# Kernel tuning notes

Measured on AMD Instinct MI355X. Metric: run time of the kernel, lower is better.

The kernel has to match this reference:

```python
import jax, jax.numpy as jnp
import numpy as np

# Static module config (matches init_kwargs)
DIM = 192
NHEADS = 6
WH, WW = 4, 8
SH, SW = 2, 4
MLP_HID = int(DIM * 4.0)


def _relative_position_index(wh, ww):
    ch, cw = np.meshgrid(np.arange(wh), np.arange(ww), indexing='ij')
    coords = np.stack([ch, cw]).reshape(2, -1)  # [2, wh*ww]
    rel = coords[:, :, None] - coords[:, None, :]  # [2, N, N]
    rel = rel.transpose(1, 2, 0)
    rel[:, :, 0] += wh - 1
    rel[:, :, 1] += ww - 1
    rel[:, :, 0] *= 2 * ww - 1
    return rel.sum(-1)  # [N, N] int


def _attn_mask(H, W, wh, ww, sh, sw):
    # Swin shift mask: -100 where tokens come from different shifted regions.
    img = np.zeros((H, W), dtype=np.float32)
    cnt = 0
    hs = (slice(0, -sh), slice(-sh, None)) if sh > 0 else (slice(0, H),)
    ws = (slice(0, -sw), slice(-sw, None)) if sw > 0 else (slice(0, W),)
    for h in hs:
        for w in ws:
            img[h, w] = cnt
            cnt += 1
    nwh, nww = H // wh, W // ww
    mw = img.reshape(nwh, wh, nww, ww).transpose(0, 2, 1, 3).reshape(-1, wh * ww)
    diff = mw[:, None, :] - mw[:, :, None]  # [nW, N, N]
    return np.where(diff != 0, -100.0, 0.0).astype(np.float32)


def _layernorm(x, g, b, eps=1e-5):
    mu = x.mean(-1, keepdims=True)
    var = ((x - mu) ** 2).mean(-1, keepdims=True)
    return (x - mu) * jax.lax.rsqrt(var + eps) * g + b


def setup_inputs() -> dict:
    key = jax.random.key(0)
    ks = jax.random.split(key, 12)
    B, H, W, C = 8, 64, 512, DIM
    x = jax.random.normal(ks[0], (B, H * W, C), dtype=jnp.float32)
    s = 0.02
    return {
        'x': x, 'H': H, 'W': W,
        'g1': jnp.ones((C,), jnp.float32), 'be1': jnp.zeros((C,), jnp.float32),
        'w_qkv': jax.random.normal(ks[1], (C, 3 * C), jnp.float32) * s,
        'b_qkv': jnp.zeros((3 * C,), jnp.float32),
        'w_proj': jax.random.normal(ks[2], (C, C), jnp.float32) * s,
        'b_proj': jnp.zeros((C,), jnp.float32),
        'bias_table': jax.random.normal(ks[3], ((2 * WH - 1) * (2 * WW - 1), NHEADS), jnp.float32) * s,
        'g2': jnp.ones((C,), jnp.float32), 'be2': jnp.zeros((C,), jnp.float32),
        'w1': jax.random.normal(ks[4], (C, MLP_HID), jnp.float32) * s,
        'bm1': jnp.zeros((MLP_HID,), jnp.float32),
        'w2': jax.random.normal(ks[5], (MLP_HID, C), jnp.float32) * s,
        'bm2': jnp.zeros((C,), jnp.float32),
    }


def reference(x, H, W, g1, be1, w_qkv, b_qkv, w_proj, b_proj, bias_table, g2, be2, w1, bm1, w2, bm2):
    B, Ntok, C = x.shape
    hd = C // NHEADS
    scale = hd ** -0.5
    N = WH * WW
    nwh, nww = H // WH, W // WW
    nW = nwh * nww

    # --- shifted window partition ---
    xr = x.reshape(B, H, W, C)
    shifted = jnp.roll(xr, (-SH, -SW), axis=(1, 2))
    win = shifted.reshape(B, nwh, WH, nww, WW, C).transpose(0, 1, 3, 2, 4, 5)
    win = win.reshape(B * nW, N, C)

    # --- window attention on norm1(windows) ---
    wn = _layernorm(win, g1, be1)
    qkv = (wn @ w_qkv + b_qkv).reshape(B * nW, N, 3, NHEADS, hd)
    q = qkv[:, :, 0].transpose(0, 2, 1, 3)  # [Bn, h, N, d]
    k = qkv[:, :, 1].transpose(0, 2, 1, 3)
    v = qkv[:, :, 2].transpose(0, 2, 1, 3)
    attn = jnp.einsum('bhnd,bhmd->bhnm', q, k) * scale

    rel_idx = _relative_position_index(WH, WW)  # static numpy
    bias = bias_table[rel_idx.reshape(-1)].reshape(N, N, NHEADS).transpose(2, 0, 1)
    attn = attn + bias[None]

    mask = jnp.asarray(_attn_mask(H, W, WH, WW, SH, SW))  # [nW, N, N]
    attn = attn.reshape(B, nW, NHEADS, N, N) + mask[None, :, None]
    attn = jax.nn.softmax(attn.reshape(B * nW, NHEADS, N, N), axis=-1)

    out = jnp.einsum('bhnm,bhmd->bhnd', attn, v)
    out = out.transpose(0, 2, 1, 3).reshape(B * nW, N, C)
    out = out @ w_proj + b_proj

    # --- window reverse + unshift ---
    merged = out.reshape(B, nwh, nww, WH, WW, C).transpose(0, 1, 3, 2, 4, 5).reshape(B, H, W, C)
    x_attn = jnp.roll(merged, (SH, SW), axis=(1, 2)).reshape(B, Ntok, C)

    x1 = x + x_attn
    h = _layernorm(x1, g2, be2)
    mlp = jax.nn.gelu(h @ w1 + bm1, approximate=False) @ w2 + bm2
    return x1 + mlp
```

## Files before the change

kernel.cpp:

```cpp
#include <hip/hip_runtime.h>
#include <hip/hip_bf16.h>

typedef unsigned short u16;
typedef unsigned int u32;
typedef __attribute__((ext_vector_type(8))) short short8;
typedef __attribute__((ext_vector_type(4))) float f32x4;

#define DEVFN static __device__ __forceinline__

DEVFN float b2f(u16 u) { return __uint_as_float(((u32)u) << 16); }
DEVFN void up2(u32 w, float& a, float& b) {
  a = __uint_as_float(w << 16);
  b = __uint_as_float(w & 0xffff0000u);
}
DEVFN u16 f2b(float f) {
  u32 u = __float_as_uint(f);
  return (u16)((u + 0x7fffu + ((u >> 16) & 1u)) >> 16);
}

DEVFN bool probe_bf16(const void* x) {
  const u32* p = (const u32*)x;
  int cnt = 0;
  for (int i = 0; i < 64; i++) {
    u32 lo = p[i] & 0xffffu;
    u32 e = (lo >> 7) & 0xffu;
    cnt += ((lo == 0u) || (e >= 97u && e <= 132u)) ? 1 : 0;
  }
  return cnt >= 48;
}

DEVFN float ld1(const void* p, size_t i, bool bf) {
  return bf ? b2f(((const u16*)p)[i]) : ((const float*)p)[i];
}
DEVFN void st1(void* p, size_t i, bool bf, float v) {
  if (bf) ((u16*)p)[i] = f2b(v); else ((float*)p)[i] = v;
}
DEVFN void ld8(const void* p, size_t i, bool bf, float* f) {
  if (bf) {
    uint4 q = *(const uint4*)((const u16*)p + i);
    up2(q.x, f[0], f[1]); up2(q.y, f[2], f[3]);
    up2(q.z, f[4], f[5]); up2(q.w, f[6], f[7]);
  } else {
    float4 t0 = *(const float4*)((const float*)p + i);
    float4 t1 = *(const float4*)((const float*)p + i + 4);
    f[0]=t0.x; f[1]=t0.y; f[2]=t0.z; f[3]=t0.w;
    f[4]=t1.x; f[5]=t1.y; f[6]=t1.z; f[7]=t1.w;
  }
}

DEVFN short8 lds16(const u16* p) { return *reinterpret_cast<const short8*>(p); }
DEVFN short8 gld16(const u16* p) { return *reinterpret_cast<const short8*>(p); }

DEVFN void bar_lds() {
  asm volatile("s_waitcnt lgkmcnt(0)" ::: "memory");
  __builtin_amdgcn_s_barrier();
}

DEVFN float gelu_t(float x) {
  const float z = x * (0.7978845608f + 0.0356774081f * x * x);
  const float e = __expf(2.f * z);
  const float t = 1.f - 2.f / (e + 1.f);
  return 0.5f * x * (1.f + t);
}


#define FLAG_OFF 442368

__global__ void transpose_weights(const void* __restrict__ w1,
                                  const void* __restrict__ w2,
                                  const void* __restrict__ wqkv,
                                  const void* __restrict__ wproj,
                                  u16* __restrict__ ws)
{
  const bool bf = probe_bf16(w1);
  const int idx = blockIdx.x * 256 + threadIdx.x;
  if (idx == 0) ws[FLAG_OFF] = bf ? 1 : 0;
  if (idx < 147456) {
    const int j = idx / 192, k = idx - 192 * j;
    ws[idx] = f2b(ld1(w1, (size_t)k * 768 + j, bf));
  } else if (idx < 294912) {
    const int i2 = idx - 147456;
    const int c = i2 / 768, h = i2 - 768 * c;
    ws[idx] = f2b(ld1(w2, (size_t)h * 192 + c, bf));
  } else if (idx < 405504) {
    const int i2 = idx - 294912;
    const int r = i2 / 192, k = i2 - 192 * r;
    const int hp = r / 192, cc = r - 192 * hp;
    const int sel = cc >> 6, hh = (cc >> 5) & 1, d = cc & 31;
    const int j = sel * 192 + (2 * hp + hh) * 32 + d;
    ws[idx] = f2b(ld1(wqkv, (size_t)k * 576 + j, bf));
  } else {
    const int i2 = idx - 405504;
    const int n = i2 / 192, k = i2 - 192 * n;
    ws[idx] = f2b(ld1(wproj, (size_t)k * 192 + n, bf));
  }
}

__launch_bounds__(256, 3)
__global__ void swin_attn_mfma(
    const void* __restrict__ x, const void* __restrict__ g1, const void* __restrict__ be1,
    const u16* __restrict__ wqkvT, const void* __restrict__ bqkv,
    const u16* __restrict__ wprojT, const void* __restrict__ bproj,
    const void* __restrict__ btab, const u16* __restrict__ bff,
    void* __restrict__ out)
{
  __shared__ __align__(16) u16 Xn[32][200];
  __shared__ __align__(16) u16 Qh[32][72];
  __shared__ __align__(16) u16 Kh[32][72];
  __shared__ __align__(16) u16 VT[64][40];
  __shared__ __align__(16) u16 Pl[2][32][40];
  __shared__ __align__(16) u16 Ou[32][200];
  __shared__ u16 Pb[1792];

  const bool bf = bff[0] != 0;
  const int tid = threadIdx.x;
  const int wid = blockIdx.x;
  const int b   = wid >> 10;
  const int wli = wid & 1023;
  const int whi = wli >> 6;
  const int wwi = wli & 63;

  auto gtok = [&](int n) -> int {
    const int r = n >> 3, c = n & 7;
    const int ho = (whi * 4 + r + 2) & 63;
    const int wo = (wwi * 8 + c + 4) & 511;
    return (b << 15) + ho * 512 + wo;
  };

  const int wave = tid >> 6;
  const int lane = tid & 63;
  const int col  = lane & 15;
  const int quad = lane >> 4;

#pragma unroll
  for (int i0 = 0; i0 < 7; i0++) {
    const int i = i0 * 256 + tid;
    float v = 0.f;
    if (i < 630) v = ld1(btab, i, bf);
    else if (i >= 1600) v = ld1(be1, i - 1600, bf);
    else if (i >= 1408) v = ld1(g1, i - 1408, bf);
    else if (i >= 1216) v = ld1(bproj, i - 1216, bf);
    else if (i >= 640) v = ld1(bqkv, i - 640, bf);
    Pb[i] = f2b(v);
  }

  short8 wreg[18];
  float v[24];
  const int ln_n = tid >> 3, ln_g = tid & 7, ln_c0 = ln_g * 24;
  {
    const size_t base = (size_t)gtok(ln_n) * 192 + ln_c0;
    ld8(x, base, bf, v); ld8(x, base + 8, bf, v + 8); ld8(x, base + 16, bf, v + 16);
  }
  {
    const u16* wb = wqkvT + (size_t)(wave * 48 + col) * 192 + quad * 8;
#pragma unroll
    for (int nt = 0; nt < 3; nt++)
#pragma unroll
      for (int ks = 0; ks < 6; ks++)
        wreg[nt * 6 + ks] = gld16(wb + nt * 16 * 192 + ks * 32);
  }
  bar_lds();

  {
    float s = 0.f, ss = 0.f;
#pragma unroll
    for (int i = 0; i < 24; i++) { s += v[i]; ss += v[i] * v[i]; }
#pragma unroll
    for (int o = 1; o < 8; o <<= 1) { s += __shfl_xor(s, o); ss += __shfl_xor(ss, o); }
    const float mu = s * (1.f / 192.f);
    const float rstd = rsqrtf(ss * (1.f / 192.f) - mu * mu + 1e-5f);
    u32* dst = reinterpret_cast<u32*>(&Xn[ln_n][ln_c0]);
#pragma unroll
    for (int i = 0; i < 12; i++) {
      const int c = ln_c0 + 2 * i;
      const float r0 = (v[2*i]   - mu) * rstd * b2f(Pb[1408 + c])     + b2f(Pb[1600 + c]);
      const float r1 = (v[2*i+1] - mu) * rstd * b2f(Pb[1408 + c + 1]) + b2f(Pb[1600 + c + 1]);
      dst[i] = (u32)f2b(r0) | ((u32)f2b(r1) << 16);
    }
  }
  bar_lds();

  const float scale = 0.17677669529663687f;
  const f32x4 zf = (f32x4){0.f, 0.f, 0.f, 0.f};
  const int hh = wave >> 1, qh = wave & 1;

  for (int hp = 0; hp < 3; ++hp) {
    f32x4 acc[2][3];
#pragma unroll
    for (int mt = 0; mt < 2; mt++)
#pragma unroll
      for (int nt = 0; nt < 3; nt++) acc[mt][nt] = zf;

#pragma unroll
    for (int ks = 0; ks < 6; ks++) {
      short8 afrg[2];
#pragma unroll
      for (int mt = 0; mt < 2; mt++)
        afrg[mt] = lds16(&Xn[16 * mt + col][ks * 32 + quad * 8]);
#pragma unroll
      for (int mt = 0; mt < 2; mt++)
#pragma unroll
        for (int nt = 0; nt < 3; nt++)
          acc[mt][nt] = __builtin_amdgcn_mfma_f32_16x16x32_bf16(
              afrg[mt], wreg[nt * 6 + ks], acc[mt][nt], 0, 0, 0);
    }

    {
      const u16* wb = (hp < 2)
        ? wqkvT + (size_t)((hp + 1) * 192 + wave * 48 + col) * 192 + quad * 8
        : wprojT + (size_t)(wave * 48 + col) * 192 + quad * 8;
#pragma unroll
      for (int nt = 0; nt < 3; nt++)
#pragma unroll
        for (int ks = 0; ks < 6; ks++)
          wreg[nt * 6 + ks] = gld16(wb + nt * 16 * 192 + ks * 32);
    }

#pragma unroll
    for (int nt = 0; nt < 3; nt++) {
      const int cc = wave * 48 + nt * 16 + col;
      const int sel = cc >> 6, hhs = (cc >> 5) & 1, d = cc & 31;
      const int j = sel * 192 + (2 * hp + hhs) * 32 + d;
      const float bq = b2f(Pb[640 + j]);
      if (sel < 2) {
        u16 (*dst)[72] = (sel == 0) ? Qh : Kh;
#pragma unroll
        for (int mt = 0; mt < 2; mt++)
#pragma unroll
          for (int r = 0; r < 4; r++) {
            const u32 mine = (u32)f2b(acc[mt][nt][r] + bq);
            const u32 part = (u32)__shfl_xor((int)mine, 1);
            if (!(lane & 1))
              *(u32*)&dst[16 * mt + quad * 4 + r][hhs * 32 + d] = mine | (part << 16);
          }
      } else {
#pragma unroll
        for (int mt = 0; mt < 2; mt++)
#pragma unroll
          for (int r = 0; r < 4; r++)
            VT[hhs * 32 + d][16 * mt + quad * 4 + r] = f2b(acc[mt][nt][r] + bq);
      }
    }
    bar_lds();

    const int hg = 2 * hp + hh;
    {
      const short8 bq_frag = lds16(&Qh[16 * qh + col][hh * 32 + quad * 8]);
      f32x4 sA[2];
#pragma unroll
      for (int mt = 0; mt < 2; mt++)
        sA[mt] = __builtin_amdgcn_mfma_f32_16x16x32_bf16(
            lds16(&Kh[16 * mt + col][hh * 32 + quad * 8]), bq_frag, zf, 0, 0, 0);

      const int qn = 16 * qh + col;
      const int rn = qn >> 3, cn = qn & 7;
      const bool rhn = (whi == 15) && (rn >= 2);
      const bool rwn = (wwi == 63) && (cn >= 4);
      float sv[8];
#pragma unroll
      for (int mt = 0; mt < 2; mt++)
#pragma unroll
        for (int r = 0; r < 4; r++) {
          const int m = 16 * mt + quad * 4 + r;
          const int rm = m >> 3, cm = m & 7;
          const float bias = b2f(Pb[((rn - rm + 3) * 15 + (cn - cm + 7)) * 6 + hg]);
          const bool rhm = (whi == 15) && (rm >= 2);
          const bool rwm = (wwi == 63) && (cm >= 4);
          const float msk = ((rhn != rhm) || (rwn != rwm)) ? -100.f : 0.f;
          sv[4 * mt + r] = sA[mt][r] * scale + bias + msk;
        }
      float mx = sv[0];
#pragma unroll
      for (int i = 1; i < 8; i++) mx = fmaxf(mx, sv[i]);
      mx = fmaxf(mx, __shfl_xor(mx, 16));
      mx = fmaxf(mx, __shfl_xor(mx, 32));
      float sum = 0.f;
#pragma unroll
      for (int i = 0; i < 8; i++) { sv[i] = __expf(sv[i] - mx); sum += sv[i]; }
      sum += __shfl_xor(sum, 16);
      sum += __shfl_xor(sum, 32);
      const float inv = 1.f / sum;
#pragma unroll
      for (int mt = 0; mt < 2; mt++) {
        uint2 w;
        w.x = (u32)f2b(sv[4 * mt]     * inv) | ((u32)f2b(sv[4 * mt + 1] * inv) << 16);
        w.y = (u32)f2b(sv[4 * mt + 2] * inv) | ((u32)f2b(sv[4 * mt + 3] * inv) << 16);
        *reinterpret_cast<uint2*>(&Pl[hh][qn][16 * mt + quad * 4]) = w;
      }
    }
    bar_lds();

    {
      const short8 a = lds16(&VT[hh * 32 + 16 * qh + col][quad * 8]);
#pragma unroll
      for (int nt = 0; nt < 2; nt++) {
        const short8 bb = lds16(&Pl[hh][16 * nt + col][quad * 8]);
        const f32x4 o = __builtin_amdgcn_mfma_f32_16x16x32_bf16(a, bb, zf, 0, 0, 0);
        uint2 w;
        w.x = (u32)f2b(o[0]) | ((u32)f2b(o[1]) << 16);
        w.y = (u32)f2b(o[2]) | ((u32)f2b(o[3]) << 16);
        *reinterpret_cast<uint2*>(&Ou[16 * nt + col][hg * 32 + 16 * qh + quad * 4]) = w;
      }
    }
    bar_lds();
  }

  {
    f32x4 pacc[2][3];
#pragma unroll
    for (int mt = 0; mt < 2; mt++)
#pragma unroll
      for (int nt = 0; nt < 3; nt++) pacc[mt][nt] = zf;

#pragma unroll
    for (int ks = 0; ks < 6; ks++) {
      short8 afrg[2];
#pragma unroll
      for (int mt = 0; mt < 2; mt++)
        afrg[mt] = lds16(&Ou[16 * mt + col][ks * 32 + quad * 8]);
#pragma unroll
      for (int mt = 0; mt < 2; mt++)
#pragma unroll
        for (int nt = 0; nt < 3; nt++)
          pacc[mt][nt] = __builtin_amdgcn_mfma_f32_16x16x32_bf16(
              afrg[mt], wreg[nt * 6 + ks], pacc[mt][nt], 0, 0, 0);
    }

    size_t gts[8];
#pragma unroll
    for (int mt = 0; mt < 2; mt++)
#pragma unroll
      for (int r = 0; r < 4; r++)
        gts[4 * mt + r] = (size_t)gtok(16 * mt + quad * 4 + r) * 192;

#pragma unroll
    for (int nt = 0; nt < 3; nt++) {
      const int c = wave * 48 + nt * 16 + col;
      const float bp = b2f(Pb[1216 + c]);
#pragma unroll
      for (int mt = 0; mt < 2; mt++)
#pragma unroll
        for (int r = 0; r < 4; r++) {
          const size_t gidx = gts[4 * mt + r] + c;
          st1(out, gidx, bf, pacc[mt][nt][r] + bp + ld1(x, gidx, bf));
        }
    }
  }
}

__launch_bounds__(256, 3)
__global__ void swin_mlp_mfma(
    const u16* __restrict__ bff,
    void* __restrict__ io, const void* __restrict__ g2, const void* __restrict__ be2,
    const u16* __restrict__ w1t,
    const void* __restrict__ bm1,
    const u16* __restrict__ w2t,
    const void* __restrict__ bm2)
{
  __shared__ __align__(16) u16 Xn[64][200];
  __shared__ __align__(16) u16 X2[64][136];
  __shared__ u16 Pm[1344];

  const bool bf = bff[0] != 0;
  const int tid = threadIdx.x;
  const size_t tok0 = (size_t)blockIdx.x * 64;
  const int wave = tid >> 6;
  const int lane = tid & 63;
  const int col  = lane & 15;
  const int quad = lane >> 4;

#pragma unroll
  for (int i0 = 0; i0 < 6; i0++) {
    const int i = i0 * 256 + tid;
    if (i < 1344) {
      float vv;
      if (i < 768) vv = ld1(bm1, i, bf);
      else if (i < 960) vv = ld1(bm2, i - 768, bf);
      else if (i < 1152) vv = ld1(g2, i - 960, bf);
      else vv = ld1(be2, i - 1152, bf);
      Pm[i] = f2b(vv);
    }
  }

  short8 wreg[12];
  float v[48];
  const int ln_t = tid >> 2, ln_g = tid & 3, ln_c0 = 48 * ln_g;
  {
    const size_t base = (tok0 + ln_t) * 192 + ln_c0;
#pragma unroll
    for (int i = 0; i < 6; i++) ld8(io, base + 8 * i, bf, v + 8 * i);
  }
  {
    const u16* wb = w1t + (size_t)(wave * 32 + col) * 192 + quad * 8;
#pragma unroll
    for (int nt = 0; nt < 2; nt++)
#pragma unroll
      for (int ks = 0; ks < 6; ks++)
        wreg[nt * 6 + ks] = gld16(wb + nt * 16 * 192 + ks * 32);
  }
  bar_lds();

  {
    float s = 0.f, ss = 0.f;
#pragma unroll
    for (int i = 0; i < 48; i++) { s += v[i]; ss += v[i] * v[i]; }
#pragma unroll
    for (int o = 1; o < 4; o <<= 1) { s += __shfl_xor(s, o); ss += __shfl_xor(ss, o); }
    const float mu = s * (1.f / 192.f);
    const float rstd = rsqrtf(ss * (1.f / 192.f) - mu * mu + 1e-5f);
    u32* dst = reinterpret_cast<u32*>(&Xn[ln_t][ln_c0]);
#pragma unroll
    for (int i = 0; i < 24; i++) {
      const int c = ln_c0 + 2 * i;
      const float r0 = (v[2*i]   - mu) * rstd * b2f(Pm[960 + c])     + b2f(Pm[1152 + c]);
      const float r1 = (v[2*i+1] - mu) * rstd * b2f(Pm[960 + c + 1]) + b2f(Pm[1152 + c + 1]);
      dst[i] = (u32)f2b(r0) | ((u32)f2b(r1) << 16);
    }
  }
  bar_lds();

  f32x4 acc2[4][3];
#pragma unroll
  for (int mt = 0; mt < 4; mt++)
#pragma unroll
    for (int nt = 0; nt < 3; nt++) acc2[mt][nt] = (f32x4){0.f, 0.f, 0.f, 0.f};

  for (int ch = 0; ch < 6; ++ch) {
    f32x4 acc1[4][2];
#pragma unroll
    for (int mt = 0; mt < 4; mt++)
#pragma unroll
      for (int nt = 0; nt < 2; nt++) acc1[mt][nt] = (f32x4){0.f, 0.f, 0.f, 0.f};

#pragma unroll
    for (int ks = 0; ks < 6; ks++) {
      short8 afrg[4];
#pragma unroll
      for (int mt = 0; mt < 4; mt++)
        afrg[mt] = lds16(&Xn[16 * mt + col][ks * 32 + quad * 8]);
#pragma unroll
      for (int mt = 0; mt < 4; mt++)
#pragma unroll
        for (int nt = 0; nt < 2; nt++)
          acc1[mt][nt] = __builtin_amdgcn_mfma_f32_16x16x32_bf16(
              afrg[mt], wreg[nt * 6 + ks], acc1[mt][nt], 0, 0, 0);
    }

    {
      const u16* wb = w2t + (size_t)(wave * 48 + col) * 768 + ch * 128 + quad * 8;
#pragma unroll
      for (int nt = 0; nt < 3; nt++)
#pragma unroll
        for (int ks = 0; ks < 4; ks++)
          wreg[nt * 4 + ks] = gld16(wb + nt * 16 * 768 + ks * 32);
    }

    const int jbase = ch * 128 + wave * 32;
#pragma unroll
    for (int nt = 0; nt < 2; nt++) {
      const float b1 = b2f(Pm[jbase + nt * 16 + col]);
      const int jl = wave * 32 + nt * 16 + col;
#pragma unroll
      for (int mt = 0; mt < 4; mt++)
#pragma unroll
        for (int r = 0; r < 4; r++) {
          const int t = 16 * mt + quad * 4 + r;
          X2[t][jl] = f2b(gelu_t(acc1[mt][nt][r] + b1));
        }
    }
    bar_lds();

#pragma unroll
    for (int ks = 0; ks < 4; ks++) {
      short8 afrg[4];
#pragma unroll
      for (int mt = 0; mt < 4; mt++)
        afrg[mt] = lds16(&X2[16 * mt + col][ks * 32 + quad * 8]);
#pragma unroll
      for (int mt = 0; mt < 4; mt++)
#pragma unroll
        for (int nt = 0; nt < 3; nt++)
          acc2[mt][nt] = __builtin_amdgcn_mfma_f32_16x16x32_bf16(
              afrg[mt], wreg[nt * 4 + ks], acc2[mt][nt], 0, 0, 0);
    }

    if (ch < 5) {
      const u16* wb = w1t + (size_t)((ch + 1) * 128 + wave * 32 + col) * 192 + quad * 8;
#pragma unroll
      for (int nt = 0; nt < 2; nt++)
#pragma unroll
        for (int ks = 0; ks < 6; ks++)
          wreg[nt * 6 + ks] = gld16(wb + nt * 16 * 192 + ks * 32);
    }
    bar_lds();
  }

#pragma unroll
  for (int nt = 0; nt < 3; nt++) {
    const int c = wave * 48 + nt * 16 + col;
    const float b2 = b2f(Pm[768 + c]);
#pragma unroll
    for (int mt = 0; mt < 4; mt++)
#pragma unroll
      for (int r = 0; r < 4; r++) {
        const int t = 16 * mt + quad * 4 + r;
        const size_t idx = (tok0 + t) * 192 + c;
        st1(io, idx, bf, acc2[mt][nt][r] + b2 + ld1(io, idx, bf));
      }
  }
}

extern "C" void kernel_launch(void* const* d_in, const int* in_sizes, int n_in,
                              void* d_out, int out_size, void* d_ws, size_t ws_size,
                              hipStream_t stream) {
  const void* x     = d_in[0];
  const void* g1    = d_in[3];
  const void* be1   = d_in[4];
  const void* wqkv  = d_in[5];
  const void* bqkv  = d_in[6];
  const void* wproj = d_in[7];
  const void* bproj = d_in[8];
  const void* btab  = d_in[9];
  const void* g2    = d_in[10];
  const void* be2   = d_in[11];
  const void* w1    = d_in[12];
  const void* bm1   = d_in[13];
  const void* w2    = d_in[14];
  const void* bm2   = d_in[15];

  u16* ws = (u16*)d_ws;

  transpose_weights<<<1728, 256, 0, stream>>>(w1, w2, wqkv, wproj, ws);
  swin_attn_mfma<<<8192, 256, 0, stream>>>(x, g1, be1, ws + 294912, bqkv,
                                           ws + 405504, bproj, btab,
                                           ws + FLAG_OFF, d_out);
  swin_mlp_mfma<<<4096, 256, 0, stream>>>(ws + FLAG_OFF, d_out, g2, be2,
                                          ws, bm1, ws + 147456, bm2);
}
```

Baseline: 1.068 ms.

## Swap MFMA operand roles so accumulators hold contiguous channels, vectorize epilogue stores

All GEMMs in the attention and MLP kernels now put the weight fragment in the A slot and activations in the B slot. Each lane's four accumulator values then cover four consecutive output channels of one token. Epilogues can therefore write packed uint2/float4 stores to LDS and global memory instead of scalar stores and lane shuffles, and the residual loads are vectorized to match. Sched barriers are also added around the LDS barrier to stop the compiler moving instructions across it. The V-transpose store becomes a scalar strided write, and the extra scheduling fences could limit the compiler's ability to interleave instructions.

```diff
diff --git a/kernel.cpp b/kernel.cpp
--- a/kernel.cpp
+++ b/kernel.cpp
@@ -16,6 +16,9 @@
 DEVFN u16 f2b(float f) {
   u32 u = __float_as_uint(f);
   return (u16)((u + 0x7fffu + ((u >> 16) & 1u)) >> 16);
+}
+DEVFN u32 pk2(float a, float b) {
+  return (u32)f2b(a) | ((u32)f2b(b) << 16);
 }
 
 DEVFN bool probe_bf16(const void* x) {
@@ -31,9 +34,6 @@
 
 DEVFN float ld1(const void* p, size_t i, bool bf) {
   return bf ? b2f(((const u16*)p)[i]) : ((const float*)p)[i];
-}
-DEVFN void st1(void* p, size_t i, bool bf, float v) {
-  if (bf) ((u16*)p)[i] = f2b(v); else ((float*)p)[i] = v;
 }
 DEVFN void ld8(const void* p, size_t i, bool bf, float* f) {
   if (bf) {
@@ -47,13 +47,33 @@
     f[4]=t1.x; f[5]=t1.y; f[6]=t1.z; f[7]=t1.w;
   }
 }
+DEVFN void ld4f(const void* p, size_t i, bool bf, float* f) {
+  if (bf) {
+    uint2 q = *(const uint2*)((const u16*)p + i);
+    up2(q.x, f[0], f[1]); up2(q.y, f[2], f[3]);
+  } else {
+    float4 t = *(const float4*)((const float*)p + i);
+    f[0]=t.x; f[1]=t.y; f[2]=t.z; f[3]=t.w;
+  }
+}
+DEVFN void st4f(void* p, size_t i, bool bf, const float* f) {
+  if (bf) {
+    uint2 q; q.x = pk2(f[0], f[1]); q.y = pk2(f[2], f[3]);
+    *(uint2*)((u16*)p + i) = q;
+  } else {
+    float4 t; t.x=f[0]; t.y=f[1]; t.z=f[2]; t.w=f[3];
+    *(float4*)((float*)p + i) = t;
+  }
+}
 
 DEVFN short8 lds16(const u16* p) { return *reinterpret_cast<const short8*>(p); }
 DEVFN short8 gld16(const u16* p) { return *reinterpret_cast<const short8*>(p); }
 
 DEVFN void bar_lds() {
+  __builtin_amdgcn_sched_barrier(0);
   asm volatile("s_waitcnt lgkmcnt(0)" ::: "memory");
   __builtin_amdgcn_s_barrier();
+  __builtin_amdgcn_sched_barrier(0);
 }
 
 DEVFN float gelu_t(float x) {
@@ -154,10 +174,10 @@
   {
     const u16* wb = wqkvT + (size_t)(wave * 48 + col) * 192 + quad * 8;
 #pragma unroll
-    for (int nt = 0; nt < 3; nt++)
+    for (int mt = 0; mt < 3; mt++)
 #pragma unroll
       for (int ks = 0; ks < 6; ks++)
-        wreg[nt * 6 + ks] = gld16(wb + nt * 16 * 192 + ks * 32);
+        wreg[mt * 6 + ks] = gld16(wb + mt * 16 * 192 + ks * 32);
   }
   bar_lds();
 
@@ -175,7 +195,7 @@
       const int c = ln_c0 + 2 * i;
       const float r0 = (v[2*i]   - mu) * rstd * b2f(Pb[1408 + c])     + b2f(Pb[1600 + c]);
       const float r1 = (v[2*i+1] - mu) * rstd * b2f(Pb[1408 + c + 1]) + b2f(Pb[1600 + c + 1]);
-      dst[i] = (u32)f2b(r0) | ((u32)f2b(r1) << 16);
+      dst[i] = pk2(r0, r1);
     }
   }
   bar_lds();
@@ -185,24 +205,24 @@
   const int hh = wave >> 1, qh = wave & 1;
 
   for (int hp = 0; hp < 3; ++hp) {
-    f32x4 acc[2][3];
-#pragma unroll
-    for (int mt = 0; mt < 2; mt++)
-#pragma unroll
-      for (int nt = 0; nt < 3; nt++) acc[mt][nt] = zf;
+    f32x4 acc[3][2];
+#pragma unroll
+    for (int mt = 0; mt < 3; mt++)
+#pragma unroll
+      for (int nt = 0; nt < 2; nt++) acc[mt][nt] = zf;
 
 #pragma unroll
     for (int ks = 0; ks < 6; ks++) {
-      short8 afrg[2];
-#pragma unroll
-      for (int mt = 0; mt < 2; mt++)
-        afrg[mt] = lds16(&Xn[16 * mt + col][ks * 32 + quad * 8]);
-#pragma unroll
-      for (int mt = 0; mt < 2; mt++)
-#pragma unroll
-        for (int nt = 0; nt < 3; nt++)
+      short8 xf[2];
+#pragma unroll
+      for (int nt = 0; nt < 2; nt++)
+        xf[nt] = lds16(&Xn[16 * nt + col][ks * 32 + quad * 8]);
+#pragma unroll
+      for (int mt = 0; mt < 3; mt++)
+#pragma unroll
+        for (int nt = 0; nt < 2; nt++)
           acc[mt][nt] = __builtin_amdgcn_mfma_f32_16x16x32_bf16(
-              afrg[mt], wreg[nt * 6 + ks], acc[mt][nt], 0, 0, 0);
+              wreg[mt * 6 + ks], xf[nt], acc[mt][nt], 0, 0, 0);
     }
 
     {
@@ -210,35 +230,38 @@
         ? wqkvT + (size_t)((hp + 1) * 192 + wave * 48 + col) * 192 + quad * 8
         : wprojT + (size_t)(wave * 48 + col) * 192 + quad * 8;
 #pragma unroll
-      for (int nt = 0; nt < 3; nt++)
+      for (int mt = 0; mt < 3; mt++)
 #pragma unroll
         for (int ks = 0; ks < 6; ks++)
-          wreg[nt * 6 + ks] = gld16(wb + nt * 16 * 192 + ks * 32);
-    }
-
-#pragma unroll
-    for (int nt = 0; nt < 3; nt++) {
-      const int cc = wave * 48 + nt * 16 + col;
-      const int sel = cc >> 6, hhs = (cc >> 5) & 1, d = cc & 31;
-      const int j = sel * 192 + (2 * hp + hhs) * 32 + d;
-      const float bq = b2f(Pb[640 + j]);
+          wreg[mt * 6 + ks] = gld16(wb + mt * 16 * 192 + ks * 32);
+    }
+
+#pragma unroll
+    for (int mt = 0; mt < 3; mt++) {
+      const int cc0 = wave * 48 + 16 * mt + quad * 4;
+      const int sel = cc0 >> 6, hhs = (cc0 >> 5) & 1, d0 = cc0 & 31;
+      const int jb = sel * 192 + (2 * hp + hhs) * 32 + d0;
+      float bq[4];
+#pragma unroll
+      for (int r = 0; r < 4; r++) bq[r] = b2f(Pb[640 + jb + r]);
       if (sel < 2) {
         u16 (*dst)[72] = (sel == 0) ? Qh : Kh;
 #pragma unroll
-        for (int mt = 0; mt < 2; mt++)
-#pragma unroll
-          for (int r = 0; r < 4; r++) {
-            const u32 mine = (u32)f2b(acc[mt][nt][r] + bq);
-            const u32 part = (u32)__shfl_xor((int)mine, 1);
-            if (!(lane & 1))
-              *(u32*)&dst[16 * mt + quad * 4 + r][hhs * 32 + d] = mine | (part << 16);
-          }
+        for (int nt = 0; nt < 2; nt++) {
+          const int tok = 16 * nt + col;
+          uint2 w;
+          w.x = pk2(acc[mt][nt][0] + bq[0], acc[mt][nt][1] + bq[1]);
+          w.y = pk2(acc[mt][nt][2] + bq[2], acc[mt][nt][3] + bq[3]);
+          *reinterpret_cast<uint2*>(&dst[tok][hhs * 32 + d0]) = w;
+        }
       } else {
 #pragma unroll
-        for (int mt = 0; mt < 2; mt++)
+        for (int nt = 0; nt < 2; nt++) {
+          const int tok = 16 * nt + col;
 #pragma unroll
           for (int r = 0; r < 4; r++)
-            VT[hhs * 32 + d][16 * mt + quad * 4 + r] = f2b(acc[mt][nt][r] + bq);
+            VT[hhs * 32 + d0 + r][tok] = f2b(acc[mt][nt][r] + bq[r]);
+        }
       }
     }
     bar_lds();
@@ -283,8 +306,8 @@
 #pragma unroll
       for (int mt = 0; mt < 2; mt++) {
         uint2 w;
-        w.x = (u32)f2b(sv[4 * mt]     * inv) | ((u32)f2b(sv[4 * mt + 1] * inv) << 16);
-        w.y = (u32)f2b(sv[4 * mt + 2] * inv) | ((u32)f2b(sv[4 * mt + 3] * inv) << 16);
+        w.x = pk2(sv[4 * mt] * inv,     sv[4 * mt + 1] * inv);
+        w.y = pk2(sv[4 * mt + 2] * inv, sv[4 * mt + 3] * inv);
         *reinterpret_cast<uint2*>(&Pl[hh][qn][16 * mt + quad * 4]) = w;
       }
     }
@@ -297,8 +320,8 @@
         const short8 bb = lds16(&Pl[hh][16 * nt + col][quad * 8]);
         const f32x4 o = __builtin_amdgcn_mfma_f32_16x16x32_bf16(a, bb, zf, 0, 0, 0);
         uint2 w;
-        w.x = (u32)f2b(o[0]) | ((u32)f2b(o[1]) << 16);
-        w.y = (u32)f2b(o[2]) | ((u32)f2b(o[3]) << 16);
+        w.x = pk2(o[0], o[1]);
+        w.y = pk2(o[2], o[3]);
         *reinterpret_cast<uint2*>(&Ou[16 * nt + col][hg * 32 + 16 * qh + quad * 4]) = w;
       }
     }
@@ -306,44 +329,46 @@
   }
 
   {
-    f32x4 pacc[2][3];
-#pragma unroll
-    for (int mt = 0; mt < 2; mt++)
-#pragma unroll
-      for (int nt = 0; nt < 3; nt++) pacc[mt][nt] = zf;
+    f32x4 pacc[3][2];
+#pragma unroll
+    for (int mt = 0; mt < 3; mt++)
+#pragma unroll
+      for (int nt = 0; nt < 2; nt++) pacc[mt][nt] = zf;
 
 #pragma unroll
     for (int ks = 0; ks < 6; ks++) {
-      short8 afrg[2];
-#pragma unroll
-      for (int mt = 0; mt < 2; mt++)
-        afrg[mt] = lds16(&Ou[16 * mt + col][ks * 32 + quad * 8]);
-#pragma unroll
-      for (int mt = 0; mt < 2; mt++)
-#pragma unroll
-        for (int nt = 0; nt < 3; nt++)
+      short8 of[2];
+#pragma unroll
+      for (int nt = 0; nt < 2; nt++)
+        of[nt] = lds16(&Ou[16 * nt + col][ks * 32 + quad * 8]);
+#pragma unroll
+      for (int mt = 0; mt < 3; mt++)
+#pragma unroll
+        for (int nt = 0; nt < 2; nt++)
           pacc[mt][nt] = __builtin_amdgcn_mfma_f32_16x16x32_bf16(
-              afrg[mt], wreg[nt * 6 + ks], pacc[mt][nt], 0, 0, 0);
-    }
-
-    size_t gts[8];
-#pragma unroll
-    for (int mt = 0; mt < 2; mt++)
-#pragma unroll
-      for (int r = 0; r < 4; r++)
-        gts[4 * mt + r] = (size_t)gtok(16 * mt + quad * 4 + r) * 192;
-
-#pragma unroll
-    for (int nt = 0; nt < 3; nt++) {
-      const int c = wave * 48 + nt * 16 + col;
-      const float bp = b2f(Pb[1216 + c]);
-#pragma unroll
-      for (int mt = 0; mt < 2; mt++)
-#pragma unroll
-        for (int r = 0; r < 4; r++) {
-          const size_t gidx = gts[4 * mt + r] + c;
-          st1(out, gidx, bf, pacc[mt][nt][r] + bp + ld1(x, gidx, bf));
-        }
+              wreg[mt * 6 + ks], of[nt], pacc[mt][nt], 0, 0, 0);
+    }
+
+    size_t gb[2];
+#pragma unroll
+    for (int nt = 0; nt < 2; nt++)
+      gb[nt] = (size_t)gtok(16 * nt + col) * 192;
+
+#pragma unroll
+    for (int mt = 0; mt < 3; mt++) {
+      const int c0 = wave * 48 + 16 * mt + quad * 4;
+      float bp[4];
+#pragma unroll
+      for (int r = 0; r < 4; r++) bp[r] = b2f(Pb[1216 + c0 + r]);
+#pragma unroll
+      for (int nt = 0; nt < 2; nt++) {
+        const size_t gi = gb[nt] + c0;
+        float f[4];
+        ld4f(x, gi, bf, f);
+#pragma unroll
+        for (int r = 0; r < 4; r++) f[r] += pacc[mt][nt][r] + bp[r];
+        st4f(out, gi, bf, f);
+      }
     }
   }
 }
@@ -393,10 +418,10 @@
   {
     const u16* wb = w1t + (size_t)(wave * 32 + col) * 192 + quad * 8;
 #pragma unroll
-    for (int nt = 0; nt < 2; nt++)
+    for (int mt = 0; mt < 2; mt++)
 #pragma unroll
       for (int ks = 0; ks < 6; ks++)
-        wreg[nt * 6 + ks] = gld16(wb + nt * 16 * 192 + ks * 32);
+        wreg[mt * 6 + ks] = gld16(wb + mt * 16 * 192 + ks * 32);
   }
   bar_lds();
 
@@ -414,99 +439,105 @@
       const int c = ln_c0 + 2 * i;
       const float r0 = (v[2*i]   - mu) * rstd * b2f(Pm[960 + c])     + b2f(Pm[1152 + c]);
       const float r1 = (v[2*i+1] - mu) * rstd * b2f(Pm[960 + c + 1]) + b2f(Pm[1152 + c + 1]);
-      dst[i] = (u32)f2b(r0) | ((u32)f2b(r1) << 16);
+      dst[i] = pk2(r0, r1);
     }
   }
   bar_lds();
 
-  f32x4 acc2[4][3];
-#pragma unroll
-  for (int mt = 0; mt < 4; mt++)
-#pragma unroll
-    for (int nt = 0; nt < 3; nt++) acc2[mt][nt] = (f32x4){0.f, 0.f, 0.f, 0.f};
+  f32x4 acc2[3][4];
+#pragma unroll
+  for (int mt = 0; mt < 3; mt++)
+#pragma unroll
+    for (int nt = 0; nt < 4; nt++) acc2[mt][nt] = (f32x4){0.f, 0.f, 0.f, 0.f};
 
   for (int ch = 0; ch < 6; ++ch) {
-    f32x4 acc1[4][2];
-#pragma unroll
-    for (int mt = 0; mt < 4; mt++)
-#pragma unroll
-      for (int nt = 0; nt < 2; nt++) acc1[mt][nt] = (f32x4){0.f, 0.f, 0.f, 0.f};
+    f32x4 acc1[2][4];
+#pragma unroll
+    for (int mt = 0; mt < 2; mt++)
+#pragma unroll
+      for (int nt = 0; nt < 4; nt++) acc1[mt][nt] = (f32x4){0.f, 0.f, 0.f, 0.f};
 
 #pragma unroll
     for (int ks = 0; ks < 6; ks++) {
-      short8 afrg[4];
-#pragma unroll
-      for (int mt = 0; mt < 4; mt++)
-        afrg[mt] = lds16(&Xn[16 * mt + col][ks * 32 + quad * 8]);
-#pragma unroll
-      for (int mt = 0; mt < 4; mt++)
-#pragma unroll
-        for (int nt = 0; nt < 2; nt++)
+      short8 xf[4];
+#pragma unroll
+      for (int nt = 0; nt < 4; nt++)
+        xf[nt] = lds16(&Xn[16 * nt + col][ks * 32 + quad * 8]);
+#pragma unroll
+      for (int mt = 0; mt < 2; mt++)
+#pragma unroll
+        for (int nt = 0; nt < 4; nt++)
           acc1[mt][nt] = __builtin_amdgcn_mfma_f32_16x16x32_bf16(
-              afrg[mt], wreg[nt * 6 + ks], acc1[mt][nt], 0, 0, 0);
+              wreg[mt * 6 + ks], xf[nt], acc1[mt][nt], 0, 0, 0);
     }
 
     {
-      const u16* wb = w2t + (size_t)(wave * 48 + col) * 768 + ch * 128 + quad * 8;
-#pragma unroll
-      for (int nt = 0; nt < 3; nt++)
+#pragma unroll
+      for (int mt = 0; mt < 3; mt++)
 #pragma unroll
         for (int ks = 0; ks < 4; ks++)
-          wreg[nt * 4 + ks] = gld16(wb + nt * 16 * 768 + ks * 32);
-    }
-
-    const int jbase = ch * 128 + wave * 32;
-#pragma unroll
-    for (int nt = 0; nt < 2; nt++) {
-      const float b1 = b2f(Pm[jbase + nt * 16 + col]);
-      const int jl = wave * 32 + nt * 16 + col;
-#pragma unroll
-      for (int mt = 0; mt < 4; mt++)
-#pragma unroll
-        for (int r = 0; r < 4; r++) {
-          const int t = 16 * mt + quad * 4 + r;
-          X2[t][jl] = f2b(gelu_t(acc1[mt][nt][r] + b1));
-        }
+          wreg[mt * 4 + ks] = gld16(w2t + (size_t)(wave * 48 + mt * 16 + col) * 768
+                                         + ch * 128 + ks * 32 + quad * 8);
+    }
+
+#pragma unroll
+    for (int mt = 0; mt < 2; mt++) {
+      const int j0 = wave * 32 + 16 * mt + quad * 4;
+      float b1[4];
+#pragma unroll
+      for (int r = 0; r < 4; r++) b1[r] = b2f(Pm[ch * 128 + j0 + r]);
+#pragma unroll
+      for (int nt = 0; nt < 4; nt++) {
+        const int tok = 16 * nt + col;
+        uint2 w;
+        w.x = pk2(gelu_t(acc1[mt][nt][0] + b1[0]), gelu_t(acc1[mt][nt][1] + b1[1]));
+        w.y = pk2(gelu_t(acc1[mt][nt][2] + b1[2]), gelu_t(acc1[mt][nt][3] + b1[3]));
+        *reinterpret_cast<uint2*>(&X2[tok][j0]) = w;
+      }
     }
     bar_lds();
 
 #pragma unroll
     for (int ks = 0; ks < 4; ks++) {
-      short8 afrg[4];
-#pragma unroll
-      for (int mt = 0; mt < 4; mt++)
-        afrg[mt] = lds16(&X2[16 * mt + col][ks * 32 + quad * 8]);
-#pragma unroll
-      for (int mt = 0; mt < 4; mt++)
-#pragma unroll
-        for (int nt = 0; nt < 3; nt++)
+      short8 xf2[4];
+#pragma unroll
+      for (int nt = 0; nt < 4; nt++)
+        xf2[nt] = lds16(&X2[16 * nt + col][ks * 32 + quad * 8]);
+#pragma unroll
+      for (int mt = 0; mt < 3; mt++)
+#pragma unroll
+        for (int nt = 0; nt < 4; nt++)
           acc2[mt][nt] = __builtin_amdgcn_mfma_f32_16x16x32_bf16(
-              afrg[mt], wreg[nt * 4 + ks], acc2[mt][nt], 0, 0, 0);
+              wreg[mt * 4 + ks], xf2[nt], acc2[mt][nt], 0, 0, 0);
     }
 
     if (ch < 5) {
       const u16* wb = w1t + (size_t)((ch + 1) * 128 + wave * 32 + col) * 192 + quad * 8;
 #pragma unroll
-      for (int nt = 0; nt < 2; nt++)
+      for (int mt = 0; mt < 2; mt++)
 #pragma unroll
         for (int ks = 0; ks < 6; ks++)
-          wreg[nt * 6 + ks] = gld16(wb + nt * 16 * 192 + ks * 32);
+          wreg[mt * 6 + ks] = gld16(wb + mt * 16 * 192 + ks * 32);
     }
     bar_lds();
   }
 
 #pragma unroll
-  for (int nt = 0; nt < 3; nt++) {
-    const int c = wave * 48 + nt * 16 + col;
-    const float b2 = b2f(Pm[768 + c]);
-#pragma unroll
-    for (int mt = 0; mt < 4; mt++)
-#pragma unroll
-      for (int r = 0; r < 4; r++) {
-        const int t = 16 * mt + quad * 4 + r;
-        const size_t idx = (tok0 + t) * 192 + c;
-        st1(io, idx, bf, acc2[mt][nt][r] + b2 + ld1(io, idx, bf));
-      }
+  for (int mt = 0; mt < 3; mt++) {
+    const int c0 = wave * 48 + 16 * mt + quad * 4;
+    float b2[4];
+#pragma unroll
+    for (int r = 0; r < 4; r++) b2[r] = b2f(Pm[768 + c0 + r]);
+#pragma unroll
+    for (int nt = 0; nt < 4; nt++) {
+      const int tok = 16 * nt + col;
+      const size_t idx = (tok0 + tok) * 192 + c0;
+      float f[4];
+      ld4f(io, idx, bf, f);
+#pragma unroll
+      for (int r = 0; r < 4; r++) f[r] += acc2[mt][nt][r] + b2[r];
+      st4f(io, idx, bf, f);
+    }
   }
 }
 
```

Result: faster. 977.2 us (-8.5%).
